# Optimization experiments

Measured on AMD Instinct MI355X. Metric: run time of the kernel, lower is better.

The kernel has to match this reference:

```python
import jax, jax.numpy as jnp
import numpy as np

N_CUST, N_PROD, D, H, OUT, E = 100000, 10000, 128, 128, 64, 500000
RELS = ["purchase", "redeem", "transfer_to", "transfer_from", "dividend_from"]


def setup_inputs() -> dict:
    key = jax.random.key(0)
    ks = jax.random.split(key, 40)
    inp = {}
    inp["x_cust"] = jax.random.normal(ks[0], (N_CUST, D), jnp.float32)
    inp["x_prod"] = jax.random.normal(ks[1], (N_PROD, D), jnp.float32)
    for i, r in enumerate(RELS):
        inp["src_" + r] = jax.random.randint(ks[2 + 2 * i], (E,), 0, N_CUST)
        inp["dst_" + r] = jax.random.randint(ks[3 + 2 * i], (E,), 0, N_PROD)
    s = 0.05
    names = [("W_gcn", (D, H)), ("b_gcn", (H,)), ("Ws_gat", (D, H)), ("Wd_gat", (D, H)),
             ("a_s_gat", (H,)), ("a_d_gat", (H,)), ("b_gat", (H,)),
             ("Wl_to", (D, H)), ("b_to", (H,)), ("Wr_to", (D, H)),
             ("Wl_from", (D, H)), ("b_from", (H,)), ("Wr_from", (D, H)),
             ("Wl_div", (D, H)), ("b_div", (H,)), ("Wr_div", (D, H)),
             ("W_out", (H, OUT)), ("b_out", (OUT,))]
    for i, (n, shp) in enumerate(names):
        inp[n] = jax.random.normal(ks[12 + i], shp, jnp.float32) * s
    return inp


def _gcn(x_src, src, dst, W, b):
    # symmetric-norm bipartite GCN: transform then gather->scale->scatter
    deg_s = jax.ops.segment_sum(jnp.ones_like(src, jnp.float32), src, N_CUST)
    deg_d = jax.ops.segment_sum(jnp.ones_like(dst, jnp.float32), dst, N_PROD)
    norm = jax.lax.rsqrt(deg_s[src] * deg_d[dst])  # [E]
    h = x_src @ W  # [N_CUST, H]
    return jax.ops.segment_sum(norm[:, None] * h[src], dst, N_PROD) + b


def _gat(x_src, x_dst, src, dst, Ws, Wd, a_s, a_d, b):
    # single-head bipartite GAT with edge-softmax over incoming edges at dst
    hs = x_src @ Ws                     # [N_CUST, H]
    ls = hs @ a_s                       # [N_CUST]
    ld = (x_dst @ Wd) @ a_d             # [N_PROD]
    logit = jax.nn.leaky_relu(ls[src] + ld[dst], 0.2)  # [E]
    m = jax.ops.segment_max(logit, dst, N_PROD)
    e = jnp.exp(logit - m[dst])
    den = jax.ops.segment_sum(e, dst, N_PROD)
    alpha = e / den[dst]
    return jax.ops.segment_sum(alpha[:, None] * hs[src], dst, N_PROD) + b


def _sage(x_src, x_dst, src, dst, Wl, bl, Wr):
    # mean-aggregate raw src features, then linear; plus root transform of dst
    s = jax.ops.segment_sum(x_src[src], dst, N_PROD)
    c = jax.ops.segment_sum(jnp.ones_like(dst, jnp.float32), dst, N_PROD)
    mean = s / jnp.maximum(c, 1.0)[:, None]
    return mean @ Wl + bl + x_dst @ Wr


def reference(x_cust, x_prod, src_purchase, dst_purchase, src_redeem, dst_redeem,
              src_transfer_to, dst_transfer_to, src_transfer_from, dst_transfer_from,
              src_dividend_from, dst_dividend_from,
              W_gcn, b_gcn, Ws_gat, Wd_gat, a_s_gat, a_d_gat, b_gat,
              Wl_to, b_to, Wr_to, Wl_from, b_from, Wr_from, Wl_div, b_div, Wr_div,
              W_out, b_out):
    prod = _gcn(x_cust, src_purchase, dst_purchase, W_gcn, b_gcn)
    prod = prod + _gat(x_cust, x_prod, src_redeem, dst_redeem, Ws_gat, Wd_gat, a_s_gat, a_d_gat, b_gat)
    prod = prod + _sage(x_cust, x_prod, src_transfer_to, dst_transfer_to, Wl_to, b_to, Wr_to)
    prod = prod + _sage(x_cust, x_prod, src_transfer_from, dst_transfer_from, Wl_from, b_from, Wr_from)
    prod = prod + _sage(x_cust, x_prod, src_dividend_from, dst_dividend_from, Wl_div, b_div, Wr_div)
    prod = jax.nn.relu(prod)  # HeteroConv(aggr='sum') then relu
    return prod @ W_out + b_out  # [N_PROD, OUT]
```

## Files before the change

kernel.cpp:

```cpp
#include <hip/hip_runtime.h>

#define WF 64
#define CAP 128
#define CH 2048
#define LC 32
#define NGMAX 160
#define BINCAP 3584

typedef int v4i __attribute__((ext_vector_type(4)));
typedef short short8 __attribute__((ext_vector_type(8)));
typedef float f32x4 __attribute__((ext_vector_type(4)));

#if __has_builtin(__builtin_amdgcn_cvt_f32_fp8) && __has_builtin(__builtin_amdgcn_cvt_pk_fp8_f32)
#define HW_FP8 1
#endif

__device__ __forceinline__ unsigned fp8enc1(float x) {
    unsigned b = __builtin_bit_cast(unsigned, x);
    unsigned s = (b >> 24) & 0x80u;
    int E = (b >> 23) & 0xff;
    unsigned m = b & 0x7fffffu;
    unsigned mr = (m + 0x7ffffu + ((m >> 20) & 1u)) >> 20;
    int e8 = E - 120 + (int)(mr >> 3);
    mr &= 7u;
    if (e8 <= 0) return s;
    if (e8 > 15) { e8 = 15; mr = 7u; }
    return s | ((unsigned)e8 << 3) | mr;
}
__device__ __forceinline__ float fp8dec1(unsigned u8) {
    unsigned f = ((u8 & 0x80u) << 24) | (((u8 & 0x7fu) << 20) + 0x3C000000u);
    return (u8 & 0x7fu) ? __builtin_bit_cast(float, f) : 0.f;
}
__device__ __forceinline__ unsigned fp8pack4(float4 u) {
#ifdef HW_FP8
    int r = __builtin_amdgcn_cvt_pk_fp8_f32(u.x, u.y, 0, false);
    r = __builtin_amdgcn_cvt_pk_fp8_f32(u.z, u.w, r, true);
    return (unsigned)r;
#else
    return fp8enc1(u.x) | (fp8enc1(u.y) << 8) | (fp8enc1(u.z) << 16) | (fp8enc1(u.w) << 24);
#endif
}
__device__ __forceinline__ void accP(float w, unsigned u,
                                     float& a0, float& a1, float& a2, float& a3) {
#ifdef HW_FP8
    a0 = fmaf(w, __builtin_amdgcn_cvt_f32_fp8((int)u, 0), a0);
    a1 = fmaf(w, __builtin_amdgcn_cvt_f32_fp8((int)u, 1), a1);
    a2 = fmaf(w, __builtin_amdgcn_cvt_f32_fp8((int)u, 2), a2);
    a3 = fmaf(w, __builtin_amdgcn_cvt_f32_fp8((int)u, 3), a3);
#else
    a0 = fmaf(w, fp8dec1(u & 0xffu), a0);
    a1 = fmaf(w, fp8dec1((u >> 8) & 0xffu), a1);
    a2 = fmaf(w, fp8dec1((u >> 16) & 0xffu), a2);
    a3 = fmaf(w, fp8dec1(u >> 24), a3);
#endif
}

__device__ __forceinline__ short bf16r(float x) {
    unsigned u = __builtin_bit_cast(unsigned, x);
    u += 0x7fffu + ((u >> 16) & 1u);
    return (short)(u >> 16);
}
__device__ __forceinline__ void bfsplit(float x, short& hi, short& lo) {
    unsigned u = __builtin_bit_cast(unsigned, x);
    hi = (short)(u >> 16);
    float fh = __builtin_bit_cast(float, u & 0xffff0000u);
    lo = bf16r(x - fh);
}

__global__ void k_init(int* deg_s, int nc2, int* bincur, int nb, int ZB,
                       const float* __restrict__ Ws, const float* __restrict__ Wd,
                       const float* __restrict__ as_, const float* __restrict__ ad_,
                       const float* __restrict__ bg, const float* __restrict__ bga,
                       const float* __restrict__ bto, const float* __restrict__ bfr,
                       const float* __restrict__ bdv,
                       const float* __restrict__ Wg, const float* __restrict__ Wlt,
                       const float* __restrict__ Wlf, const float* __restrict__ Wld,
                       const float* __restrict__ Wrt, const float* __restrict__ Wrf,
                       const float* __restrict__ Wrd, const float* __restrict__ Wo,
                       float* vs, float* vd, float* bsum,
                       short* wth, short* wtl, short* woth, short* wotl) {
    int b = blockIdx.x, t = threadIdx.x;
    if (b < ZB) {
        int i = b * 256 + t;
        if (i < nc2) deg_s[i] = 0;
        if (i < nb) bincur[i] = 0;
    } else if (b == ZB) {
        if (t < 128) {
            float a = 0.f, bb = 0.f;
            for (int h = 0; h < 128; ++h) {
                a += Ws[t * 128 + h] * as_[h];
                bb += Wd[t * 128 + h] * ad_[h];
            }
            vs[t] = a; vd[t] = bb;
            bsum[t] = bg[t] + bga[t] + bto[t] + bfr[t] + bdv[t];
        }
    } else if (b < ZB + 385) {
        int e = (b - ZB - 1) * 256 + t;
        int h = e / 768;
        int q = e - h * 768;
        int m = q >> 7, k = q & 127;
        int src = k * 128 + h;
        float val;
        switch (m) {
            case 0: val = Wg[src]; break;
            case 1: val = Ws[src]; break;
            case 2: val = Wlt[src]; break;
            case 3: val = Wlf[src]; break;
            case 4: val = Wld[src]; break;
            default: val = Wrt[src] + Wrf[src] + Wrd[src]; break;
        }
        short hi, lo;
        bfsplit(val, hi, lo);
        wth[e] = hi; wtl[e] = lo;
    } else {
        int e = (b - ZB - 385) * 256 + t;
        int o = e >> 7, k = e & 127;
        short hi, lo;
        bfsplit(Wo[k * 64 + o], hi, lo);
        woth[e] = hi; wotl[e] = lo;
    }
}

__global__ __launch_bounds__(256) void k_bin(
    const int* s0, const int* s1, const int* s2, const int* s3, const int* s4,
    const int* d0, const int* d1, const int* d2, const int* d3, const int* d4,
    int* bincur, int* gbin, int* deg_s, int E, int NP, int ng,
    int bpjE, int B0, int HB4, int CB,
    const float* __restrict__ xc, const float* __restrict__ xp,
    const float* __restrict__ vs, const float* __restrict__ vd,
    unsigned* __restrict__ xh, float* __restrict__ lsb, float* __restrict__ ldb,
    int NC) {
    __shared__ int lcnt[NGMAX];
    __shared__ int lbase[NGMAX];
    __shared__ int lbin[NGMAX * LC];
    int b = blockIdx.x, t = threadIdx.x;
    if (b < B0) {
        int rel = b / bpjE;
        int blk = b - rel * bpjE;
        const int *sp, *dp;
        switch (rel) {
            case 0: sp = s0; dp = d0; break;
            case 1: sp = s1; dp = d1; break;
            case 2: sp = s2; dp = d2; break;
            case 3: sp = s3; dp = d3; break;
            default: sp = s4; dp = d4; break;
        }
        for (int i = t; i < ng; i += 256) lcnt[i] = 0;
        __syncthreads();
        int* bc = bincur + rel * ng;
        int* gb0 = gbin + (size_t)rel * ng * BINCAP;
        int start = blk * CH;
        int q0 = start + t * 8;
#pragma unroll
        for (int c = 0; c < 8; c += 4) {
            int q = q0 + c;
            if (q >= E) break;
            if (q + 3 < E) {
                v4i dv = __builtin_nontemporal_load((const v4i*)(dp + q));
                v4i sv = __builtin_nontemporal_load((const v4i*)(sp + q));
                int dd[4] = {dv.x, dv.y, dv.z, dv.w};
                int ss[4] = {sv.x, sv.y, sv.z, sv.w};
#pragma unroll
                for (int z = 0; z < 4; ++z) {
                    int bin = dd[z] >> 6;
                    int pk = (ss[z] << 6) | (dd[z] & 63);
                    int pos = atomicAdd(&lcnt[bin], 1);
                    if (pos < LC) lbin[bin * LC + pos] = pk;
                    else {
                        int g = atomicAdd(bc + bin, 1);
                        if (g < BINCAP) gb0[(size_t)bin * BINCAP + g] = pk;
                    }
                }
            } else {
                for (int i = q; i < E; ++i) {
                    int d = dp[i];
                    int bin = d >> 6;
                    int pk = (sp[i] << 6) | (d & 63);
                    int pos = atomicAdd(&lcnt[bin], 1);
                    if (pos < LC) lbin[bin * LC + pos] = pk;
                    else {
                        int g = atomicAdd(bc + bin, 1);
                        if (g < BINCAP) gb0[(size_t)bin * BINCAP + g] = pk;
                    }
                }
            }
        }
        __syncthreads();
        if (t < ng) {
            int c = min(lcnt[t], LC);
            lbase[t] = atomicAdd(bc + t, c);
        }
        __syncthreads();
        int wv = t >> 6, lane = t & 63;
        for (int bin = wv; bin < ng; bin += 4) {
            int c = min(lcnt[bin], LC);
            int gbase = lbase[bin];
            int* gp = gb0 + (size_t)bin * BINCAP;
            for (int i = lane; i < c; i += 64) {
                int g = gbase + i;
                if (g < BINCAP) gp[g] = lbin[bin * LC + i];
            }
        }
    } else if (b < B0 + HB4) {
        int q = ((b - B0) * 256 + t) * 4;
        if (q >= E) return;
        if (q + 3 < E) {
            v4i v = __builtin_nontemporal_load((const v4i*)(s0 + q));
            atomicAdd(deg_s + v.x, 1); atomicAdd(deg_s + v.y, 1);
            atomicAdd(deg_s + v.z, 1); atomicAdd(deg_s + v.w, 1);
        } else {
            for (int i = q; i < E; ++i) atomicAdd(deg_s + s0[i], 1);
        }
    } else if (b < B0 + HB4 + CB) {
        int row = (b - B0 - HB4) * 8 + (t >> 5);
        int q = t & 31;
        if (row >= NC) return;
        float4 u = *(const float4*)(xc + (size_t)row * 128 + 4 * q);
        float4 v = *(const float4*)(vs + 4 * q);
        float s = u.x * v.x + u.y * v.y + u.z * v.z + u.w * v.w;
        xh[(size_t)row * 32 + q] = fp8pack4(u);
#pragma unroll
        for (int o = 16; o; o >>= 1) s += __shfl_xor(s, o, WF);
        if (q == 0) lsb[row] = s;
    } else {
        int row = (b - B0 - HB4 - CB) * 4 + (t >> 6);
        int l = t & 63;
        if (row >= NP) return;
        const float* xr = xp + (size_t)row * 128;
        float s = xr[2 * l] * vd[2 * l] + xr[2 * l + 1] * vd[2 * l + 1];
        for (int o = 32; o; o >>= 1) s += __shfl_down(s, o, WF);
        if (l == 0) ldb[row] = s;
    }
}

__global__ __launch_bounds__(256) void k_aggf(
    const int* __restrict__ gbin, const int* __restrict__ bincur,
    const int* __restrict__ deg_s,
    const float* __restrict__ ls, const float* __restrict__ ld,
    const unsigned* __restrict__ xh,
    float* __restrict__ aggG, float* __restrict__ aggA, float* __restrict__ aggM,
    int NP, int ng) {
    __shared__ int cnt[16];
    __shared__ int buck[16][CAP + 1];
    __shared__ float wbuf[4][CAP + 1];
    int t = threadIdx.x;
    int rel = blockIdx.x / (4 * ng);
    int rem = blockIdx.x - rel * 4 * ng;
    int grp = rem >> 2, sub = rem & 3;
    if (t < 16) cnt[t] = 0;
    __syncthreads();
    int binid = rel * ng + grp;
    int n = min(bincur[binid], BINCAP);
    const int* bsrc = gbin + (size_t)binid * BINCAP;
    for (int i = t; i < n; i += 256) {
        int e = bsrc[i];
        int lp = e & 63;
        if ((lp >> 4) == sub) {
            int li = lp & 15;
            int pos = atomicAdd(&cnt[li], 1);
            if (pos < CAP) buck[li][pos] = e >> 6;
        }
    }
    __syncthreads();
    if (t < 16) buck[t][min(cnt[t], CAP)] = 0;
    __syncthreads();

    int wv = t >> 6, l = t & 63;
    int half = l >> 5, q = l & 31;

    for (int r = 0; r < 4; ++r) {
        int li = r * 4 + wv;
        int p = grp * 64 + sub * 16 + li;
        bool valid = (p < NP);
        int m = valid ? min(cnt[li], CAP) : 0;

        if (rel == 0) {
            float rd = rsqrtf((float)m);
            for (int e = l; e < m; e += WF)
                wbuf[wv][e] = rsqrtf((float)deg_s[buck[li][e]]) * rd;
        } else if (rel == 1) {
            if (m > 0) {
                float ldp = ld[p];
                float ml = -3.4e38f, dl = 0.f;
                for (int e = l; e < m; e += WF) {
                    float tt = ls[buck[li][e]] + ldp;
                    tt = tt > 0.f ? tt : 0.2f * tt;
                    wbuf[wv][e] = tt;
                    if (tt > ml) { dl = dl * __expf(ml - tt) + 1.f; ml = tt; }
                    else dl += __expf(tt - ml);
                }
                for (int o = 32; o; o >>= 1) {
                    float m2 = __shfl_xor(ml, o, WF), d2 = __shfl_xor(dl, o, WF);
                    float mm = fmaxf(ml, m2);
                    dl = dl * __expf(ml - mm) + d2 * __expf(m2 - mm);
                    ml = mm;
                }
                float inv = 1.f / dl;
                for (int e = l; e < m; e += WF)
                    wbuf[wv][e] = __expf(wbuf[wv][e] - ml) * inv;
            }
        } else {
            float sc = 1.f / fmaxf((float)m, 1.f);
            for (int e = l; e < m; e += WF) wbuf[wv][e] = sc;
        }
        if (l == 0) wbuf[wv][m] = 0.f;
        __builtin_amdgcn_wave_barrier();

        float a0 = 0.f, a1 = 0.f, a2 = 0.f, a3 = 0.f;
        int npairs = (m + 1) >> 1;
        int j = 0;
        for (; j + 8 <= npairs; j += 8) {
            int ss[8]; float wk[8]; unsigned uu[8];
#pragma unroll
            for (int z = 0; z < 8; ++z) {
                int e = 2 * (j + z) + half;
                ss[z] = buck[li][e];
                wk[z] = wbuf[wv][e];
            }
#pragma unroll
            for (int z = 0; z < 8; ++z)
                uu[z] = xh[(size_t)ss[z] * 32 + q];
#pragma unroll
            for (int z = 0; z < 8; ++z)
                accP(wk[z], uu[z], a0, a1, a2, a3);
        }
        for (; j < npairs; ++j) {
            int e = 2 * j + half;
            int s0 = buck[li][e];
            float w0 = wbuf[wv][e];
            unsigned u0 = xh[(size_t)s0 * 32 + q];
            accP(w0, u0, a0, a1, a2, a3);
        }

        a0 += __shfl_xor(a0, 32, WF);
        a1 += __shfl_xor(a1, 32, WF);
        a2 += __shfl_xor(a2, 32, WF);
        a3 += __shfl_xor(a3, 32, WF);

        if (valid && l < 32) {
            float* dst;
            if (rel == 0)      dst = aggG + (size_t)p * 128;
            else if (rel == 1) dst = aggA + (size_t)p * 128;
            else               dst = aggM + ((size_t)(rel - 2) * NP + p) * 128;
            *(float4*)(dst + 4 * q) = make_float4(a0, a1, a2, a3);
        }
    }
}

__global__ __launch_bounds__(256) void k_gemm_out(
    const float* __restrict__ A0, const float* __restrict__ A1, const float* __restrict__ A2,
    const float* __restrict__ A3, const float* __restrict__ A4, const float* __restrict__ A5,
    const short* __restrict__ wth, const short* __restrict__ wtl,
    const short* __restrict__ woth, const short* __restrict__ wotl,
    const float* __restrict__ bsum, const float* __restrict__ bout,
    float* __restrict__ out, int NP) {
    __shared__ short c1h[32][136];
    __shared__ short c1l[32][136];
    int t = threadIdx.x;
    int w = t >> 6, l = t & 63;
    int wr = w >> 1, wc = w & 1;
    int lr = l & 15, lq = l >> 4;
    int kq = lq * 8;
    int row0 = blockIdx.x * 32;
    const float* Af[6] = {A0, A1, A2, A3, A4, A5};

    f32x4 acc[4] = {};
    int ar = row0 + 16 * wr + lr;
    if (ar > NP - 1) ar = NP - 1;

#pragma unroll
    for (int m = 0; m < 6; ++m) {
        const float* ap = Af[m] + (size_t)ar * 128;
#pragma unroll
        for (int kk = 0; kk < 4; ++kk) {
            int koff = kk * 32 + kq;
            float4 u0 = *(const float4*)(ap + koff);
            float4 u1 = *(const float4*)(ap + koff + 4);
            float uf[8] = {u0.x, u0.y, u0.z, u0.w, u1.x, u1.y, u1.z, u1.w};
            short8 ah, al;
#pragma unroll
            for (int j = 0; j < 8; ++j) {
                short hh, ll;
                bfsplit(uf[j], hh, ll);
                ah[j] = hh; al[j] = ll;
            }
            int kbase = m * 128 + kk * 32 + kq;
#pragma unroll
            for (int ci = 0; ci < 4; ++ci) {
                int hcol = 64 * wc + 16 * ci + lr;
                short8 bh = *(const short8*)(wth + (size_t)hcol * 768 + kbase);
                short8 bl = *(const short8*)(wtl + (size_t)hcol * 768 + kbase);
                acc[ci] = __builtin_amdgcn_mfma_f32_16x16x32_bf16(ah, bh, acc[ci], 0, 0, 0);
                acc[ci] = __builtin_amdgcn_mfma_f32_16x16x32_bf16(al, bh, acc[ci], 0, 0, 0);
                acc[ci] = __builtin_amdgcn_mfma_f32_16x16x32_bf16(ah, bl, acc[ci], 0, 0, 0);
            }
        }
    }

#pragma unroll
    for (int ci = 0; ci < 4; ++ci) {
        int col = 64 * wc + 16 * ci + lr;
        float bs = bsum[col];
#pragma unroll
        for (int r = 0; r < 4; ++r) {
            float v = acc[ci][r] + bs;
            v = v > 0.f ? v : 0.f;
            short hh, ll;
            bfsplit(v, hh, ll);
            int rl = 16 * wr + 4 * lq + r;
            c1h[rl][col] = hh;
            c1l[rl][col] = ll;
        }
    }
    __syncthreads();

    f32x4 acc2[2] = {};
    int r16 = 16 * (w >> 1);
    int oc0 = 32 * (w & 1);
#pragma unroll
    for (int kb2 = 0; kb2 < 4; ++kb2) {
        int kof = kb2 * 32 + kq;
        short8 a2h = *(const short8*)&c1h[r16 + lr][kof];
        short8 a2l = *(const short8*)&c1l[r16 + lr][kof];
#pragma unroll
        for (int nb = 0; nb < 2; ++nb) {
            int o = oc0 + 16 * nb + lr;
            short8 b2h = *(const short8*)(woth + o * 128 + kof);
            short8 b2l = *(const short8*)(wotl + o * 128 + kof);
            acc2[nb] = __builtin_amdgcn_mfma_f32_16x16x32_bf16(a2h, b2h, acc2[nb], 0, 0, 0);
            acc2[nb] = __builtin_amdgcn_mfma_f32_16x16x32_bf16(a2l, b2h, acc2[nb], 0, 0, 0);
            acc2[nb] = __builtin_amdgcn_mfma_f32_16x16x32_bf16(a2h, b2l, acc2[nb], 0, 0, 0);
        }
    }
#pragma unroll
    for (int nb = 0; nb < 2; ++nb) {
        int col = oc0 + 16 * nb + lr;
        float bo = bout[col];
#pragma unroll
        for (int r = 0; r < 4; ++r) {
            int row = row0 + r16 + 4 * lq + r;
            if (row < NP) out[(size_t)row * 64 + col] = acc2[nb][r] + bo;
        }
    }
}

extern "C" void kernel_launch(void* const* d_in, const int* in_sizes, int n_in,
                              void* d_out, int out_size, void* d_ws, size_t ws_size,
                              hipStream_t stream) {
    const float* x_cust = (const float*)d_in[0];
    const float* x_prod = (const float*)d_in[1];
    const int* src_pur = (const int*)d_in[2];  const int* dst_pur = (const int*)d_in[3];
    const int* src_red = (const int*)d_in[4];  const int* dst_red = (const int*)d_in[5];
    const int* src_to  = (const int*)d_in[6];  const int* dst_to  = (const int*)d_in[7];
    const int* src_fr  = (const int*)d_in[8];  const int* dst_fr  = (const int*)d_in[9];
    const int* src_dv  = (const int*)d_in[10]; const int* dst_dv  = (const int*)d_in[11];
    const float* W_gcn = (const float*)d_in[12];
    const float* b_gcn = (const float*)d_in[13];
    const float* Ws_gat = (const float*)d_in[14]; const float* Wd_gat = (const float*)d_in[15];
    const float* a_s = (const float*)d_in[16]; const float* a_d = (const float*)d_in[17];
    const float* b_gat = (const float*)d_in[18];
    const float* Wl_to = (const float*)d_in[19]; const float* b_to = (const float*)d_in[20];
    const float* Wr_to = (const float*)d_in[21];
    const float* Wl_fr = (const float*)d_in[22]; const float* b_fr = (const float*)d_in[23];
    const float* Wr_fr = (const float*)d_in[24];
    const float* Wl_dv = (const float*)d_in[25]; const float* b_dv = (const float*)d_in[26];
    const float* Wr_dv = (const float*)d_in[27];
    const float* W_out = (const float*)d_in[28]; const float* b_out = (const float*)d_in[29];
    float* out = (float*)d_out;

    int NC = in_sizes[0] / 128;
    int NP = in_sizes[1] / 128;
    int E  = in_sizes[2];
    int ng = (NP + 63) >> 6;

    char* ws = (char*)d_ws;
    size_t off = 0;
    auto alloc = [&](size_t bytes) -> void* {
        void* p = ws + off;
        off = (off + bytes + 255) & ~(size_t)255;
        return p;
    };
    int*      deg_s  = (int*)alloc((size_t)NC * 4);
    int*      bincur = (int*)alloc((size_t)5 * NGMAX * 4);
    int*      gbin   = (int*)alloc((size_t)5 * NGMAX * BINCAP * 4);
    float*    lsb    = (float*)alloc((size_t)NC * 4);
    float*    ldb    = (float*)alloc((size_t)NP * 4);
    float*    vs     = (float*)alloc(512);
    float*    vd     = (float*)alloc(512);
    float*    bsum   = (float*)alloc(512);
    short*    wth    = (short*)alloc((size_t)98304 * 2);
    short*    wtl    = (short*)alloc((size_t)98304 * 2);
    short*    woth   = (short*)alloc((size_t)8192 * 2);
    short*    wotl   = (short*)alloc((size_t)8192 * 2);
    unsigned* xh     = (unsigned*)alloc((size_t)NC * 32 * 4);
    float*    aggG   = (float*)alloc((size_t)5 * NP * 128 * 4);
    float*    aggA   = aggG + (size_t)NP * 128;
    float*    aggM   = aggG + (size_t)2 * NP * 128;

    int ZB = (NC + 255) / 256;
    k_init<<<ZB + 1 + 384 + 32, 256, 0, stream>>>(deg_s, NC, bincur, 5 * ng, ZB,
                                                  Ws_gat, Wd_gat, a_s, a_d,
                                                  b_gcn, b_gat, b_to, b_fr, b_dv,
                                                  W_gcn, Wl_to, Wl_fr, Wl_dv,
                                                  Wr_to, Wr_fr, Wr_dv, W_out,
                                                  vs, vd, bsum, wth, wtl, woth, wotl);

    int bpjE = (E + CH - 1) / CH;
    int bpj4 = ((E + 3) / 4 + 255) / 256;
    int B0 = 5 * bpjE, HB4 = bpj4, CB = (NC + 7) / 8, PB = (NP + 3) / 4;
    k_bin<<<B0 + HB4 + CB + PB, 256, 0, stream>>>(
        src_pur, src_red, src_to, src_fr, src_dv,
        dst_pur, dst_red, dst_to, dst_fr, dst_dv,
        bincur, gbin, deg_s, E, NP, ng, bpjE, B0, HB4, CB,
        x_cust, x_prod, vs, vd, xh, lsb, ldb, NC);

    k_aggf<<<5 * ng * 4, 256, 0, stream>>>(gbin, bincur, deg_s, lsb, ldb, xh,
                                           aggG, aggA, aggM, NP, ng);

    k_gemm_out<<<(NP + 31) / 32, 256, 0, stream>>>(
        aggG, aggA, aggM, aggM + (size_t)NP * 128, aggM + (size_t)2 * NP * 128, x_prod,
        wth, wtl, woth, wotl, bsum, b_out, out, NP);
}
```

Measured before the change: 305.7 us.

## Store aggregates as split bf16 hi/lo and retile output GEMM to 16 rows

After: 298.2 us. 1.03x faster.

```diff
diff --git a/kernel.cpp b/kernel.cpp
--- a/kernel.cpp
+++ b/kernel.cpp
@@ -9,6 +9,7 @@
 
 typedef int v4i __attribute__((ext_vector_type(4)));
 typedef short short8 __attribute__((ext_vector_type(8)));
+typedef short s16x4 __attribute__((ext_vector_type(4)));
 typedef float f32x4 __attribute__((ext_vector_type(4)));
 
 #if __has_builtin(__builtin_amdgcn_cvt_f32_fp8) && __has_builtin(__builtin_amdgcn_cvt_pk_fp8_f32)
@@ -129,7 +130,7 @@
     const float* __restrict__ xc, const float* __restrict__ xp,
     const float* __restrict__ vs, const float* __restrict__ vd,
     unsigned* __restrict__ xh, float* __restrict__ lsb, float* __restrict__ ldb,
-    int NC) {
+    short* __restrict__ xph, short* __restrict__ xpl, int NC) {
     __shared__ int lcnt[NGMAX];
     __shared__ int lbase[NGMAX];
     __shared__ int lbin[NGMAX * LC];
@@ -227,7 +228,15 @@
         int l = t & 63;
         if (row >= NP) return;
         const float* xr = xp + (size_t)row * 128;
-        float s = xr[2 * l] * vd[2 * l] + xr[2 * l + 1] * vd[2 * l + 1];
+        float x0 = xr[2 * l], x1 = xr[2 * l + 1];
+        short h0, lo0, h1, lo1;
+        bfsplit(x0, h0, lo0);
+        bfsplit(x1, h1, lo1);
+        ((unsigned*)(xph + (size_t)row * 128))[l] =
+            (unsigned)(unsigned short)h0 | ((unsigned)(unsigned short)h1 << 16);
+        ((unsigned*)(xpl + (size_t)row * 128))[l] =
+            (unsigned)(unsigned short)lo0 | ((unsigned)(unsigned short)lo1 << 16);
+        float s = x0 * vd[2 * l] + x1 * vd[2 * l + 1];
         for (int o = 32; o; o >>= 1) s += __shfl_down(s, o, WF);
         if (l == 0) ldb[row] = s;
     }
@@ -238,7 +247,7 @@
     const int* __restrict__ deg_s,
     const float* __restrict__ ls, const float* __restrict__ ld,
     const unsigned* __restrict__ xh,
-    float* __restrict__ aggG, float* __restrict__ aggA, float* __restrict__ aggM,
+    short* __restrict__ aggH, short* __restrict__ aggL,
     int NP, int ng) {
     __shared__ int cnt[16];
     __shared__ int buck[16][CAP + 1];
@@ -338,56 +347,50 @@
         a3 += __shfl_xor(a3, 32, WF);
 
         if (valid && l < 32) {
-            float* dst;
-            if (rel == 0)      dst = aggG + (size_t)p * 128;
-            else if (rel == 1) dst = aggA + (size_t)p * 128;
-            else               dst = aggM + ((size_t)(rel - 2) * NP + p) * 128;
-            *(float4*)(dst + 4 * q) = make_float4(a0, a1, a2, a3);
-        }
-    }
-}
-
-__global__ __launch_bounds__(256) void k_gemm_out(
-    const float* __restrict__ A0, const float* __restrict__ A1, const float* __restrict__ A2,
-    const float* __restrict__ A3, const float* __restrict__ A4, const float* __restrict__ A5,
+            s16x4 hv, lv;
+            short hh, ll;
+            bfsplit(a0, hh, ll); hv[0] = hh; lv[0] = ll;
+            bfsplit(a1, hh, ll); hv[1] = hh; lv[1] = ll;
+            bfsplit(a2, hh, ll); hv[2] = hh; lv[2] = ll;
+            bfsplit(a3, hh, ll); hv[3] = hh; lv[3] = ll;
+            size_t base = ((size_t)rel * NP + p) * 128 + 4 * q;
+            *(s16x4*)(aggH + base) = hv;
+            *(s16x4*)(aggL + base) = lv;
+        }
+    }
+}
+
+__global__ __launch_bounds__(256, 2) void k_gemm_out(
+    const short* __restrict__ aggH, const short* __restrict__ aggL,
     const short* __restrict__ wth, const short* __restrict__ wtl,
     const short* __restrict__ woth, const short* __restrict__ wotl,
     const float* __restrict__ bsum, const float* __restrict__ bout,
     float* __restrict__ out, int NP) {
-    __shared__ short c1h[32][136];
-    __shared__ short c1l[32][136];
+    __shared__ short c1h[16][136];
+    __shared__ short c1l[16][136];
     int t = threadIdx.x;
     int w = t >> 6, l = t & 63;
-    int wr = w >> 1, wc = w & 1;
     int lr = l & 15, lq = l >> 4;
     int kq = lq * 8;
-    int row0 = blockIdx.x * 32;
-    const float* Af[6] = {A0, A1, A2, A3, A4, A5};
-
-    f32x4 acc[4] = {};
-    int ar = row0 + 16 * wr + lr;
+    int row0 = blockIdx.x * 16;
+    int ar = row0 + lr;
     if (ar > NP - 1) ar = NP - 1;
 
+    f32x4 acc[2] = {};
+
 #pragma unroll
     for (int m = 0; m < 6; ++m) {
-        const float* ap = Af[m] + (size_t)ar * 128;
+        const short* ahp = aggH + ((size_t)m * NP + ar) * 128;
+        const short* alp = aggL + ((size_t)m * NP + ar) * 128;
 #pragma unroll
         for (int kk = 0; kk < 4; ++kk) {
-            int koff = kk * 32 + kq;
-            float4 u0 = *(const float4*)(ap + koff);
-            float4 u1 = *(const float4*)(ap + koff + 4);
-            float uf[8] = {u0.x, u0.y, u0.z, u0.w, u1.x, u1.y, u1.z, u1.w};
-            short8 ah, al;
-#pragma unroll
-            for (int j = 0; j < 8; ++j) {
-                short hh, ll;
-                bfsplit(uf[j], hh, ll);
-                ah[j] = hh; al[j] = ll;
-            }
-            int kbase = m * 128 + kk * 32 + kq;
-#pragma unroll
-            for (int ci = 0; ci < 4; ++ci) {
-                int hcol = 64 * wc + 16 * ci + lr;
+            int ko = kk * 32 + kq;
+            short8 ah = *(const short8*)(ahp + ko);
+            short8 al = *(const short8*)(alp + ko);
+            int kbase = m * 128 + ko;
+#pragma unroll
+            for (int ci = 0; ci < 2; ++ci) {
+                int hcol = 32 * w + 16 * ci + lr;
                 short8 bh = *(const short8*)(wth + (size_t)hcol * 768 + kbase);
                 short8 bl = *(const short8*)(wtl + (size_t)hcol * 768 + kbase);
                 acc[ci] = __builtin_amdgcn_mfma_f32_16x16x32_bf16(ah, bh, acc[ci], 0, 0, 0);
@@ -398,8 +401,8 @@
     }
 
 #pragma unroll
-    for (int ci = 0; ci < 4; ++ci) {
-        int col = 64 * wc + 16 * ci + lr;
+    for (int ci = 0; ci < 2; ++ci) {
+        int col = 32 * w + 16 * ci + lr;
         float bs = bsum[col];
 #pragma unroll
         for (int r = 0; r < 4; ++r) {
@@ -407,40 +410,32 @@
             v = v > 0.f ? v : 0.f;
             short hh, ll;
             bfsplit(v, hh, ll);
-            int rl = 16 * wr + 4 * lq + r;
+            int rl = 4 * lq + r;
             c1h[rl][col] = hh;
             c1l[rl][col] = ll;
         }
     }
     __syncthreads();
 
-    f32x4 acc2[2] = {};
-    int r16 = 16 * (w >> 1);
-    int oc0 = 32 * (w & 1);
-#pragma unroll
-    for (int kb2 = 0; kb2 < 4; ++kb2) {
-        int kof = kb2 * 32 + kq;
-        short8 a2h = *(const short8*)&c1h[r16 + lr][kof];
-        short8 a2l = *(const short8*)&c1l[r16 + lr][kof];
-#pragma unroll
-        for (int nb = 0; nb < 2; ++nb) {
-            int o = oc0 + 16 * nb + lr;
-            short8 b2h = *(const short8*)(woth + o * 128 + kof);
-            short8 b2l = *(const short8*)(wotl + o * 128 + kof);
-            acc2[nb] = __builtin_amdgcn_mfma_f32_16x16x32_bf16(a2h, b2h, acc2[nb], 0, 0, 0);
-            acc2[nb] = __builtin_amdgcn_mfma_f32_16x16x32_bf16(a2l, b2h, acc2[nb], 0, 0, 0);
-            acc2[nb] = __builtin_amdgcn_mfma_f32_16x16x32_bf16(a2h, b2l, acc2[nb], 0, 0, 0);
-        }
-    }
-#pragma unroll
-    for (int nb = 0; nb < 2; ++nb) {
-        int col = oc0 + 16 * nb + lr;
-        float bo = bout[col];
-#pragma unroll
-        for (int r = 0; r < 4; ++r) {
-            int row = row0 + r16 + 4 * lq + r;
-            if (row < NP) out[(size_t)row * 64 + col] = acc2[nb][r] + bo;
-        }
+    f32x4 acc2 = {};
+#pragma unroll
+    for (int kb = 0; kb < 4; ++kb) {
+        int kof = kb * 32 + kq;
+        short8 a2h = *(const short8*)&c1h[lr][kof];
+        short8 a2l = *(const short8*)&c1l[lr][kof];
+        int o = 16 * w + lr;
+        short8 b2h = *(const short8*)(woth + o * 128 + kof);
+        short8 b2l = *(const short8*)(wotl + o * 128 + kof);
+        acc2 = __builtin_amdgcn_mfma_f32_16x16x32_bf16(a2h, b2h, acc2, 0, 0, 0);
+        acc2 = __builtin_amdgcn_mfma_f32_16x16x32_bf16(a2l, b2h, acc2, 0, 0, 0);
+        acc2 = __builtin_amdgcn_mfma_f32_16x16x32_bf16(a2h, b2l, acc2, 0, 0, 0);
+    }
+    int col = 16 * w + lr;
+    float bo = bout[col];
+#pragma unroll
+    for (int r = 0; r < 4; ++r) {
+        int row = row0 + 4 * lq + r;
+        if (row < NP) out[(size_t)row * 64 + col] = acc2[r] + bo;
     }
 }
 
@@ -493,9 +488,10 @@
     short*    woth   = (short*)alloc((size_t)8192 * 2);
     short*    wotl   = (short*)alloc((size_t)8192 * 2);
     unsigned* xh     = (unsigned*)alloc((size_t)NC * 32 * 4);
-    float*    aggG   = (float*)alloc((size_t)5 * NP * 128 * 4);
-    float*    aggA   = aggG + (size_t)NP * 128;
-    float*    aggM   = aggG + (size_t)2 * NP * 128;
+    short*    aggH   = (short*)alloc((size_t)6 * NP * 128 * 2);
+    short*    aggL   = (short*)alloc((size_t)6 * NP * 128 * 2);
+    short*    xph    = aggH + (size_t)5 * NP * 128;
+    short*    xpl    = aggL + (size_t)5 * NP * 128;
 
     int ZB = (NC + 255) / 256;
     k_init<<<ZB + 1 + 384 + 32, 256, 0, stream>>>(deg_s, NC, bincur, 5 * ng, ZB,
@@ -512,12 +508,11 @@
         src_pur, src_red, src_to, src_fr, src_dv,
         dst_pur, dst_red, dst_to, dst_fr, dst_dv,
         bincur, gbin, deg_s, E, NP, ng, bpjE, B0, HB4, CB,
-        x_cust, x_prod, vs, vd, xh, lsb, ldb, NC);
+        x_cust, x_prod, vs, vd, xh, lsb, ldb, xph, xpl, NC);
 
     k_aggf<<<5 * ng * 4, 256, 0, stream>>>(gbin, bincur, deg_s, lsb, ldb, xh,
-                                           aggG, aggA, aggM, NP, ng);
-
-    k_gemm_out<<<(NP + 31) / 32, 256, 0, stream>>>(
-        aggG, aggA, aggM, aggM + (size_t)NP * 128, aggM + (size_t)2 * NP * 128, x_prod,
-        wth, wtl, woth, wotl, bsum, b_out, out, NP);
-}
+                                           aggH, aggL, NP, ng);
+
+    k_gemm_out<<<(NP + 15) / 16, 256, 0, stream>>>(
+        aggH, aggL, wth, wtl, woth, wotl, bsum, b_out, out, NP);
+}
```
